# Optimization experiments

Measured on AMD Instinct MI355X. Metric: run time of the kernel, lower is better.

Reference implementation:

```python
import jax, jax.numpy as jnp
import numpy as np

HEADS = 8


def setup_inputs() -> dict:
    key = jax.random.key(0)
    ks = jax.random.split(key, 9)
    B, C, H, W = 16, 512, 32, 32
    d = C // HEADS
    scale = d ** -0.5
    return {
        "x": jax.random.normal(ks[0], (B, C, H, W), dtype=jnp.float32),
        "Wq": jax.random.normal(ks[1], (C, C), dtype=jnp.float32) * (C ** -0.5),
        "bq": jax.random.normal(ks[2], (C,), dtype=jnp.float32) * 0.02,
        "Wk": jax.random.normal(ks[3], (C, C), dtype=jnp.float32) * (C ** -0.5),
        "bk": jax.random.normal(ks[4], (C,), dtype=jnp.float32) * 0.02,
        "Wv": jax.random.normal(ks[5], (C, C), dtype=jnp.float32) * (C ** -0.5),
        "bv": jax.random.normal(ks[6], (C,), dtype=jnp.float32) * 0.02,
        "rel_h": jax.random.normal(ks[7], (d, H, 1), dtype=jnp.float32) * scale,
        "rel_w": jax.random.normal(ks[8], (d, 1, W), dtype=jnp.float32) * scale,
    }


def reference(x, Wq, bq, Wk, bk, Wv, bv, rel_h, rel_w):
    B, C, H, W = x.shape
    heads = HEADS
    d = C // heads
    scale = d ** -0.5
    N = H * W
    xf = x.reshape(B, C, N)  # 1x1 conv == per-pixel linear over channels
    q = (jnp.einsum('oc,bcn->bon', Wq, xf) + bq[:, None]).reshape(B, heads, d, N)
    k = (jnp.einsum('oc,bcn->bon', Wk, xf) + bk[:, None]).reshape(B, heads, d, N)
    v = (jnp.einsum('oc,bcn->bon', Wv, xf) + bv[:, None]).reshape(B, heads, d, N)
    q = q * scale
    # content-content scores [B, heads, N, N]
    cc = jnp.einsum('bhdi,bhdj->bhij', q, k)
    # relative position bias table [d, N], projected by q
    cp_tab = (rel_h + rel_w).reshape(d, N)
    cp = jnp.einsum('bhdi,dj->bhij', q, cp_tab)
    beta = jax.nn.softmax(cc + cp, axis=-1)
    attn = jnp.einsum('bhij,bhdj->bhid', beta, v)  # [B, heads, N, d]
    # original does .view(x.shape) on [b,h,i,d] -> keep same raw reshape
    return attn.reshape(B, C, H, W)
```

## Files before the change

kernel.cpp:

```cpp
#include <hip/hip_runtime.h>
#include <hip/hip_bf16.h>
#include <stdint.h>

typedef unsigned short u16;
typedef u16 u16x8 __attribute__((ext_vector_type(8)));
typedef u16 u16x4 __attribute__((ext_vector_type(4)));
typedef __bf16 bf16x8 __attribute__((ext_vector_type(8)));
typedef float f32x4 __attribute__((ext_vector_type(4)));

#define MFMA16(a, b, c) __builtin_amdgcn_mfma_f32_16x16x32_bf16((a), (b), (c), 0, 0, 0)

#define SCALE_Q 0.18033688011112042f

__device__ __forceinline__ u16 f2b(float f) {
    union { float f; unsigned u; } v; v.f = f;
    unsigned r = v.u + 0x7FFFu + ((v.u >> 16) & 1u);
    return (u16)(r >> 16);
}
__device__ __forceinline__ u16 f2b_h(float f) {
    union { float f; unsigned u; } v; v.f = f;
    return (u16)((v.u + 0x8000u) >> 16);
}

__device__ __forceinline__ void gload16(const u16* g, u16* l) {
    __builtin_amdgcn_global_load_lds(
        (const __attribute__((address_space(1))) unsigned int*)g,
        (__attribute__((address_space(3))) unsigned int*)l, 16, 0, 0);
}

__global__ __launch_bounds__(256) void prep(
    const float* __restrict__ x,
    const float* __restrict__ Wq, const float* __restrict__ Wk,
    const float* __restrict__ Wv,
    u16* __restrict__ wb, u16* __restrict__ xT) {
    __shared__ __align__(16) u16 Ls[128 * 72];
    const int tid = threadIdx.x;

    if (blockIdx.x < 384) {
        int g = blockIdx.x * 256 + tid;
        int which = g >> 15;
        const float* src = which == 0 ? Wq : (which == 1 ? Wk : Wv);
        int off = (g & 32767) * 8;
        f32x4 a = *(const f32x4*)(src + off);
        f32x4 b = *(const f32x4*)(src + off + 4);
        u16x8 o;
#pragma unroll
        for (int i = 0; i < 4; ++i) { o[i] = f2b_h(a[i]); o[4 + i] = f2b_h(b[i]); }
        *(u16x8*)(wb + (size_t)g * 8) = o;
        return;
    }

    const int bid = blockIdx.x - 384;
    const int b  = bid >> 6;
    const int ct = (bid >> 3) & 7;
    const int nt = bid & 7;
    const int C0 = ct * 64, N0 = nt * 128;
    const float* xb = x + ((size_t)b << 19);

#pragma unroll
    for (int rep = 0; rep < 4; ++rep) {
        int id = tid + rep * 256;
        int oct = id >> 7, n = id & 127;
        const float* xp = xb + (size_t)(C0 + oct * 8) * 1024 + N0 + n;
        u16x8 xv;
#pragma unroll
        for (int k = 0; k < 8; ++k) xv[k] = f2b_h(xp[k * 1024]);
        *(u16x8*)(Ls + n * 72 + oct * 8) = xv;
    }
    __syncthreads();
#pragma unroll
    for (int rep = 0; rep < 4; ++rep) {
        int id = tid + rep * 256;
        int n = id >> 3, c8 = id & 7;
        *(u16x8*)(xT + ((size_t)b << 19) + (size_t)(N0 + n) * 512 + C0 + c8 * 8) =
            *(u16x8*)(Ls + n * 72 + c8 * 8);
    }
}

__global__ __launch_bounds__(256, 3) void qkv_proj(
    const u16* __restrict__ xT, const u16* __restrict__ wb,
    const float* __restrict__ bq, const float* __restrict__ bk,
    const float* __restrict__ bv,
    const float* __restrict__ rel_h, const float* __restrict__ rel_w,
    u16* __restrict__ qws, u16* __restrict__ kws, u16* __restrict__ vws) {
    __shared__ __align__(16) u16 Xs[128 * 72];
    __shared__ __align__(16) u16 Ws[128 * 72];

    const int tid  = threadIdx.x;
    const int wave = tid >> 6, lane = tid & 63;
    const int quad = lane >> 4, l16 = lane & 15;
    const int wr = wave >> 1, wc = wave & 1;

    const int id = blockIdx.x;
    const int nt = id & 7;
    const int r  = id >> 3;
    const int o0 = r & 3;
    const int r2 = r >> 2;
    const int mm = r2 % 3;
    const int b  = r2 / 3;
    const int N0 = nt * 128;
    const int O0 = o0 * 128;

    const u16*   W    = wb + (size_t)mm * 262144;
    const float* bias = mm == 0 ? bq : (mm == 1 ? bk : bv);
    const u16*   Xb   = xT + ((size_t)b << 19);

    const int sr = tid >> 3, sc8 = tid & 7;

    u16x8 xr[4], wrg[4];
#pragma unroll
    for (int rp = 0; rp < 4; ++rp) {
        xr[rp]  = *(const u16x8*)(Xb + (size_t)(N0 + sr + rp * 32) * 512 + sc8 * 8);
        wrg[rp] = *(const u16x8*)(W  + (size_t)(O0 + sr + rp * 32) * 512 + sc8 * 8);
    }

    f32x4 acc[4][4] = {};

    for (int kt = 0; kt < 8; ++kt) {
        __syncthreads();
#pragma unroll
        for (int rp = 0; rp < 4; ++rp) {
            *(u16x8*)(Xs + (sr + rp * 32) * 72 + sc8 * 8) = xr[rp];
            *(u16x8*)(Ws + (sr + rp * 32) * 72 + sc8 * 8) = wrg[rp];
        }
        __syncthreads();
        if (kt < 7) {
            int c0 = (kt + 1) * 64;
#pragma unroll
            for (int rp = 0; rp < 4; ++rp) {
                xr[rp]  = *(const u16x8*)(Xb + (size_t)(N0 + sr + rp * 32) * 512 + c0 + sc8 * 8);
                wrg[rp] = *(const u16x8*)(W  + (size_t)(O0 + sr + rp * 32) * 512 + c0 + sc8 * 8);
            }
        }
#pragma unroll
        for (int kk = 0; kk < 2; ++kk) {
            bf16x8 af[4], bfr[4];
#pragma unroll
            for (int mi = 0; mi < 4; ++mi)
                af[mi] = *(bf16x8*)(Xs + (wr * 64 + mi * 16 + l16) * 72 + kk * 32 + quad * 8);
#pragma unroll
            for (int ni = 0; ni < 4; ++ni)
                bfr[ni] = *(bf16x8*)(Ws + (wc * 64 + ni * 16 + l16) * 72 + kk * 32 + quad * 8);
#pragma unroll
            for (int mi = 0; mi < 4; ++mi)
#pragma unroll
                for (int ni = 0; ni < 4; ++ni)
                    acc[mi][ni] = MFMA16(af[mi], bfr[ni], acc[mi][ni]);
        }
    }

#pragma unroll
    for (int mi = 0; mi < 4; ++mi) {
#pragma unroll
        for (int ni = 0; ni < 4; ++ni) {
            int o  = O0 + wc * 64 + ni * 16 + l16;
            int h  = o >> 6, dd = o & 63;
            size_t bh = (size_t)b * 8 + h;
            float bv_ = bias[o];
            int n0 = N0 + wr * 64 + mi * 16 + quad * 4;
            if (mm == 2) {
                u16x4 pk;
#pragma unroll
                for (int rr = 0; rr < 4; ++rr) pk[rr] = f2b(acc[mi][ni][rr] + bv_);
                int qq = (n0 >> 2) & 3, ss = (n0 >> 4) & 1;
                int np = (n0 & ~31) | (qq * 8 + ss * 4);
                int slot = ((np >> 3) & 7) ^ (dd & 7);
                int np2 = (np & ~63) | (slot << 3) | (np & 7);
                *(u16x4*)(vws + (bh * 64 + dd) * 1024 + np2) = pk;
            } else if (mm == 0) {
#pragma unroll
                for (int rr = 0; rr < 4; ++rr)
                    qws[(bh * 1024 + (n0 + rr)) * 64 + dd] =
                        f2b((acc[mi][ni][rr] + bv_) * SCALE_Q);
            } else {
                float th = rel_h[dd * 32 + (n0 >> 5)];
                f32x4 tw = *(const f32x4*)(rel_w + dd * 32 + (n0 & 31));
#pragma unroll
                for (int rr = 0; rr < 4; ++rr) {
                    int n = n0 + rr;
                    int sdd = (((dd >> 3) ^ (n & 7)) << 3) | (dd & 7);
                    kws[(bh * 1024 + n) * 64 + sdd] =
                        f2b(acc[mi][ni][rr] + bv_ + th + tw[rr]);
                }
            }
        }
    }
}

__global__ __launch_bounds__(512, 6) void attn(
    const u16* __restrict__ qws, const u16* __restrict__ kws,
    const u16* __restrict__ vws, float* __restrict__ out) {
    __shared__ __align__(16) u16 KPb[2][64 * 64];
    __shared__ __align__(16) u16 Vtb[2][64 * 64];

    const int tid  = threadIdx.x;
    const int wave = tid >> 6, lane = tid & 63;
    const int quad = lane >> 4, l16 = lane & 15;
    const int id = blockIdx.x;
    const int h  = id & 7;
    const int qt = (id >> 3) & 7;
    const int b  = id >> 6;
    const size_t bh = (size_t)b * 8 + h;

    const u16* Q = qws + (bh * 1024 + (size_t)qt * 128) * 64;
    const u16* K = kws + bh * 65536;
    const u16* V = vws + bh * 65536;

    const int lrow = wave * 8 + (lane >> 3);
    const int lc8  = lane & 7;
    const u16* Kl = K + (size_t)lrow * 64 + lc8 * 8;
    const u16* Vl = V + ((size_t)lrow << 10) + lc8 * 8;
    u16* const KP0 = &KPb[0][0];
    u16* const Vt0 = &Vtb[0][0];
    const int wofs = wave * 512;

    bf16x8 qf[2];
#pragma unroll
    for (int ks = 0; ks < 2; ++ks)
        qf[ks] = *(const bf16x8*)(Q + (wave * 16 + l16) * 64 + ks * 32 + quad * 8);

    const int xsw = (l16 & 7) << 4;
    const int xk0 = (quad * 16) ^ xsw;
    const int xk1 = (64 + quad * 16) ^ xsw;

    f32x4 accO[4] = {};
    f32x4 s4 = {};

    gload16(Kl, KP0 + wofs);
    gload16(Vl, Vt0 + wofs);

    auto body = [&](int jt, int cur) {
        __syncthreads();
        if (jt < 15) {
            int nxt = cur ^ 1;
            gload16(Kl + (jt + 1) * 4096, KP0 + nxt * 4096 + wofs);
            gload16(Vl + (jt + 1) * 64,  Vt0 + nxt * 4096 + wofs);
        }
        const char* KP = (const char*)(KP0 + cur * 4096);
        const char* Vt = (const char*)(Vt0 + cur * 4096);

        f32x4 accST[4] = {};
#pragma unroll
        for (int ks = 0; ks < 2; ++ks) {
            const int xo = ks ? xk1 : xk0;
            bf16x8 kf[4];
#pragma unroll
            for (int mj = 0; mj < 4; ++mj)
                kf[mj] = *(const bf16x8*)(KP + (mj * 16 + l16) * 128 + xo);
            __builtin_amdgcn_s_setprio(1);
#pragma unroll
            for (int mj = 0; mj < 4; ++mj)
                accST[mj] = MFMA16(kf[mj], qf[ks], accST[mj]);
            __builtin_amdgcn_s_setprio(0);
        }

#pragma unroll
        for (int mj = 0; mj < 4; ++mj) {
            f32x4 p;
#pragma unroll
            for (int rr = 0; rr < 4; ++rr)
                p[rr] = __builtin_amdgcn_exp2f(accST[mj][rr]);
            s4 += p;
            accST[mj] = p;
        }

#pragma unroll
        for (int ks2 = 0; ks2 < 2; ++ks2) {
            union { u16x8 u; bf16x8 b; } pfr;
            u16x8 t;
#pragma unroll
            for (int rr = 0; rr < 4; ++rr) {
                t[rr]     = f2b_h(accST[2 * ks2][rr]);
                t[4 + rr] = f2b_h(accST[2 * ks2 + 1][rr]);
            }
            pfr.u = t;
            const int xo = ks2 ? xk1 : xk0;
            bf16x8 vf[4];
#pragma unroll
            for (int md = 0; md < 4; ++md)
                vf[md] = *(const bf16x8*)(Vt + (md * 16 + l16) * 128 + xo);
            __builtin_amdgcn_s_setprio(1);
#pragma unroll
            for (int md = 0; md < 4; ++md)
                accO[md] = MFMA16(vf[md], pfr.b, accO[md]);
            __builtin_amdgcn_s_setprio(0);
        }
    };

    for (int j2 = 0; j2 < 8; ++j2) {
        body(2 * j2,     0);
        body(2 * j2 + 1, 1);
    }

    float rs = (s4[0] + s4[1]) + (s4[2] + s4[3]);
    rs += __shfl_xor(rs, 16);
    rs += __shfl_xor(rs, 32);
    float inv = 1.0f / rs;
    int i = qt * 128 + wave * 16 + l16;
#pragma unroll
    for (int md = 0; md < 4; ++md) {
        f32x4 pk;
#pragma unroll
        for (int rr = 0; rr < 4; ++rr) pk[rr] = accO[md][rr] * inv;
        *(f32x4*)(out + (bh * 1024 + i) * 64 + md * 16 + quad * 4) = pk;
    }
}

extern "C" void kernel_launch(void* const* d_in, const int* in_sizes, int n_in,
                              void* d_out, int out_size, void* d_ws, size_t ws_size,
                              hipStream_t stream) {
    const float* x  = (const float*)d_in[0];
    const float* Wq = (const float*)d_in[1];
    const float* bq = (const float*)d_in[2];
    const float* Wk = (const float*)d_in[3];
    const float* bk = (const float*)d_in[4];
    const float* Wv = (const float*)d_in[5];
    const float* bv = (const float*)d_in[6];
    const float* rh = (const float*)d_in[7];
    const float* rw = (const float*)d_in[8];
    float* out = (float*)d_out;

    u16* kws = (u16*)d_ws;
    u16* vws = kws + 8388608;
    u16* qws = vws + 8388608;
    u16* wb  = qws + 8388608;
    u16* xT  = (u16*)d_out;

    prep<<<1408, 256, 0, stream>>>(x, Wq, Wk, Wv, wb, xT);
    qkv_proj<<<1536, 256, 0, stream>>>(xT, wb, bq, bk, bv, rh, rw, qws, kws, vws);
    attn<<<1024, 512, 0, stream>>>(qws, kws, vws, out);
}
```

Before: 185.0 us.

## Double-buffer QKV GEMM via direct-to-LDS loads and double attention query tile

The QKV projection now streams 32-wide K slices straight into double-buffered, swizzled LDS with global_load_lds, replacing the register-staged copy and dropping one barrier per step. Its occupancy hint rises from 3 to 4 blocks. The attention kernel gives each wave 32 query rows instead of 16, so every K/V tile loaded into LDS is reused twice and the grid halves. P is packed to bf16 with the hardware v_cvt_pk_bf16_f32 instruction. The cost is higher register pressure in attn (occupancy hint lowered to 4) and fewer blocks to fill the GPU.

```diff
diff --git a/kernel.cpp b/kernel.cpp
--- a/kernel.cpp
+++ b/kernel.cpp
@@ -5,6 +5,7 @@
 typedef unsigned short u16;
 typedef u16 u16x8 __attribute__((ext_vector_type(8)));
 typedef u16 u16x4 __attribute__((ext_vector_type(4)));
+typedef unsigned int u32x4 __attribute__((ext_vector_type(4)));
 typedef __bf16 bf16x8 __attribute__((ext_vector_type(8)));
 typedef float f32x4 __attribute__((ext_vector_type(4)));
 
@@ -20,6 +21,11 @@
 __device__ __forceinline__ u16 f2b_h(float f) {
     union { float f; unsigned u; } v; v.f = f;
     return (u16)((v.u + 0x8000u) >> 16);
+}
+__device__ __forceinline__ unsigned pk2(float lo, float hi) {
+    unsigned r;
+    asm("v_cvt_pk_bf16_f32 %0, %1, %2" : "=v"(r) : "v"(lo), "v"(hi));
+    return r;
 }
 
 __device__ __forceinline__ void gload16(const u16* g, u16* l) {
@@ -77,14 +83,14 @@
     }
 }
 
-__global__ __launch_bounds__(256, 3) void qkv_proj(
+__global__ __launch_bounds__(256, 4) void qkv_proj(
     const u16* __restrict__ xT, const u16* __restrict__ wb,
     const float* __restrict__ bq, const float* __restrict__ bk,
     const float* __restrict__ bv,
     const float* __restrict__ rel_h, const float* __restrict__ rel_w,
     u16* __restrict__ qws, u16* __restrict__ kws, u16* __restrict__ vws) {
-    __shared__ __align__(16) u16 Xs[128 * 72];
-    __shared__ __align__(16) u16 Ws[128 * 72];
+    __shared__ __align__(16) u16 Xs2[2][128 * 32];
+    __shared__ __align__(16) u16 Ws2[2][128 * 32];
 
     const int tid  = threadIdx.x;
     const int wave = tid >> 6, lane = tid & 63;
@@ -105,48 +111,50 @@
     const float* bias = mm == 0 ? bq : (mm == 1 ? bk : bv);
     const u16*   Xb   = xT + ((size_t)b << 19);
 
-    const int sr = tid >> 3, sc8 = tid & 7;
-
-    u16x8 xr[4], wrg[4];
-#pragma unroll
-    for (int rp = 0; rp < 4; ++rp) {
-        xr[rp]  = *(const u16x8*)(Xb + (size_t)(N0 + sr + rp * 32) * 512 + sc8 * 8);
-        wrg[rp] = *(const u16x8*)(W  + (size_t)(O0 + sr + rp * 32) * 512 + sc8 * 8);
-    }
+    const int srow = wave * 16 + (lane >> 2);
+    const int sl   = ((lane & 3) ^ (lane >> 4)) * 8;
+    const u16* Xg = Xb + (size_t)(N0 + srow) * 512 + sl;
+    const u16* Wg = W  + (size_t)(O0 + srow) * 512 + sl;
+    u16* const XL = &Xs2[0][0];
+    u16* const WL = &Ws2[0][0];
+    const int wofs = wave * 512;
+
+    auto STAGE = [&](int kt, int buf) {
+        gload16(Xg + kt * 32,         XL + buf * 4096 + wofs);
+        gload16(Xg + kt * 32 + 32768, XL + buf * 4096 + 2048 + wofs);
+        gload16(Wg + kt * 32,         WL + buf * 4096 + wofs);
+        gload16(Wg + kt * 32 + 32768, WL + buf * 4096 + 2048 + wofs);
+    };
 
     f32x4 acc[4][4] = {};
-
-    for (int kt = 0; kt < 8; ++kt) {
+    const int fsl = (quad ^ (l16 >> 2)) * 8;
+
+    STAGE(0, 0);
+
+    auto step = [&](int kt, int cur) {
         __syncthreads();
-#pragma unroll
-        for (int rp = 0; rp < 4; ++rp) {
-            *(u16x8*)(Xs + (sr + rp * 32) * 72 + sc8 * 8) = xr[rp];
-            *(u16x8*)(Ws + (sr + rp * 32) * 72 + sc8 * 8) = wrg[rp];
-        }
-        __syncthreads();
-        if (kt < 7) {
-            int c0 = (kt + 1) * 64;
-#pragma unroll
-            for (int rp = 0; rp < 4; ++rp) {
-                xr[rp]  = *(const u16x8*)(Xb + (size_t)(N0 + sr + rp * 32) * 512 + c0 + sc8 * 8);
-                wrg[rp] = *(const u16x8*)(W  + (size_t)(O0 + sr + rp * 32) * 512 + c0 + sc8 * 8);
-            }
-        }
-#pragma unroll
-        for (int kk = 0; kk < 2; ++kk) {
-            bf16x8 af[4], bfr[4];
-#pragma unroll
-            for (int mi = 0; mi < 4; ++mi)
-                af[mi] = *(bf16x8*)(Xs + (wr * 64 + mi * 16 + l16) * 72 + kk * 32 + quad * 8);
+        if (kt < 15) STAGE(kt + 1, cur ^ 1);
+        const u16* Xc = XL + cur * 4096;
+        const u16* Wc = WL + cur * 4096;
+        bf16x8 af[4], bfr[4];
+#pragma unroll
+        for (int mi = 0; mi < 4; ++mi)
+            af[mi] = *(const bf16x8*)(Xc + (wr * 64 + mi * 16 + l16) * 32 + fsl);
+#pragma unroll
+        for (int ni = 0; ni < 4; ++ni)
+            bfr[ni] = *(const bf16x8*)(Wc + (wc * 64 + ni * 16 + l16) * 32 + fsl);
+        __builtin_amdgcn_s_setprio(1);
+#pragma unroll
+        for (int mi = 0; mi < 4; ++mi)
 #pragma unroll
             for (int ni = 0; ni < 4; ++ni)
-                bfr[ni] = *(bf16x8*)(Ws + (wc * 64 + ni * 16 + l16) * 72 + kk * 32 + quad * 8);
-#pragma unroll
-            for (int mi = 0; mi < 4; ++mi)
-#pragma unroll
-                for (int ni = 0; ni < 4; ++ni)
-                    acc[mi][ni] = MFMA16(af[mi], bfr[ni], acc[mi][ni]);
-        }
+                acc[mi][ni] = MFMA16(af[mi], bfr[ni], acc[mi][ni]);
+        __builtin_amdgcn_s_setprio(0);
+    };
+
+    for (int k2 = 0; k2 < 8; ++k2) {
+        step(2 * k2,     0);
+        step(2 * k2 + 1, 1);
     }
 
 #pragma unroll
@@ -187,7 +195,7 @@
     }
 }
 
-__global__ __launch_bounds__(512, 6) void attn(
+__global__ __launch_bounds__(512, 4) void attn(
     const u16* __restrict__ qws, const u16* __restrict__ kws,
     const u16* __restrict__ vws, float* __restrict__ out) {
     __shared__ __align__(16) u16 KPb[2][64 * 64];
@@ -198,11 +206,11 @@
     const int quad = lane >> 4, l16 = lane & 15;
     const int id = blockIdx.x;
     const int h  = id & 7;
-    const int qt = (id >> 3) & 7;
-    const int b  = id >> 6;
+    const int qt = (id >> 3) & 3;
+    const int b  = id >> 5;
     const size_t bh = (size_t)b * 8 + h;
 
-    const u16* Q = qws + (bh * 1024 + (size_t)qt * 128) * 64;
+    const u16* Q = qws + (bh * 1024 + (size_t)qt * 256) * 64;
     const u16* K = kws + bh * 65536;
     const u16* V = vws + bh * 65536;
 
@@ -214,17 +222,19 @@
     u16* const Vt0 = &Vtb[0][0];
     const int wofs = wave * 512;
 
-    bf16x8 qf[2];
-#pragma unroll
-    for (int ks = 0; ks < 2; ++ks)
-        qf[ks] = *(const bf16x8*)(Q + (wave * 16 + l16) * 64 + ks * 32 + quad * 8);
+    bf16x8 qf[2][2];
+#pragma unroll
+    for (int ni = 0; ni < 2; ++ni)
+#pragma unroll
+        for (int ks = 0; ks < 2; ++ks)
+            qf[ni][ks] = *(const bf16x8*)(Q + (wave * 32 + ni * 16 + l16) * 64 + ks * 32 + quad * 8);
 
     const int xsw = (l16 & 7) << 4;
     const int xk0 = (quad * 16) ^ xsw;
     const int xk1 = (64 + quad * 16) ^ xsw;
 
-    f32x4 accO[4] = {};
-    f32x4 s4 = {};
+    f32x4 accO[4][2] = {};
+    f32x4 s4[2] = {};
 
     gload16(Kl, KP0 + wofs);
     gload16(Vl, Vt0 + wofs);
@@ -239,7 +249,7 @@
         const char* KP = (const char*)(KP0 + cur * 4096);
         const char* Vt = (const char*)(Vt0 + cur * 4096);
 
-        f32x4 accST[4] = {};
+        f32x4 aST[4][2] = {};
 #pragma unroll
         for (int ks = 0; ks < 2; ++ks) {
             const int xo = ks ? xk1 : xk0;
@@ -250,30 +260,34 @@
             __builtin_amdgcn_s_setprio(1);
 #pragma unroll
             for (int mj = 0; mj < 4; ++mj)
-                accST[mj] = MFMA16(kf[mj], qf[ks], accST[mj]);
+#pragma unroll
+                for (int ni = 0; ni < 2; ++ni)
+                    aST[mj][ni] = MFMA16(kf[mj], qf[ni][ks], aST[mj][ni]);
             __builtin_amdgcn_s_setprio(0);
         }
 
 #pragma unroll
-        for (int mj = 0; mj < 4; ++mj) {
-            f32x4 p;
-#pragma unroll
-            for (int rr = 0; rr < 4; ++rr)
-                p[rr] = __builtin_amdgcn_exp2f(accST[mj][rr]);
-            s4 += p;
-            accST[mj] = p;
-        }
+        for (int mj = 0; mj < 4; ++mj)
+#pragma unroll
+            for (int ni = 0; ni < 2; ++ni) {
+                f32x4 p;
+#pragma unroll
+                for (int rr = 0; rr < 4; ++rr)
+                    p[rr] = __builtin_amdgcn_exp2f(aST[mj][ni][rr]);
+                s4[ni] += p;
+                aST[mj][ni] = p;
+            }
 
 #pragma unroll
         for (int ks2 = 0; ks2 < 2; ++ks2) {
-            union { u16x8 u; bf16x8 b; } pfr;
-            u16x8 t;
-#pragma unroll
-            for (int rr = 0; rr < 4; ++rr) {
-                t[rr]     = f2b_h(accST[2 * ks2][rr]);
-                t[4 + rr] = f2b_h(accST[2 * ks2 + 1][rr]);
+            union { u32x4 u; bf16x8 b; } pfr[2];
+#pragma unroll
+            for (int ni = 0; ni < 2; ++ni) {
+                pfr[ni].u[0] = pk2(aST[2 * ks2][ni][0],     aST[2 * ks2][ni][1]);
+                pfr[ni].u[1] = pk2(aST[2 * ks2][ni][2],     aST[2 * ks2][ni][3]);
+                pfr[ni].u[2] = pk2(aST[2 * ks2 + 1][ni][0], aST[2 * ks2 + 1][ni][1]);
+                pfr[ni].u[3] = pk2(aST[2 * ks2 + 1][ni][2], aST[2 * ks2 + 1][ni][3]);
             }
-            pfr.u = t;
             const int xo = ks2 ? xk1 : xk0;
             bf16x8 vf[4];
 #pragma unroll
@@ -282,7 +296,9 @@
             __builtin_amdgcn_s_setprio(1);
 #pragma unroll
             for (int md = 0; md < 4; ++md)
-                accO[md] = MFMA16(vf[md], pfr.b, accO[md]);
+#pragma unroll
+                for (int ni = 0; ni < 2; ++ni)
+                    accO[md][ni] = MFMA16(vf[md], pfr[ni].b, accO[md][ni]);
             __builtin_amdgcn_s_setprio(0);
         }
     };
@@ -292,17 +308,20 @@
         body(2 * j2 + 1, 1);
     }
 
-    float rs = (s4[0] + s4[1]) + (s4[2] + s4[3]);
-    rs += __shfl_xor(rs, 16);
-    rs += __shfl_xor(rs, 32);
-    float inv = 1.0f / rs;
-    int i = qt * 128 + wave * 16 + l16;
-#pragma unroll
-    for (int md = 0; md < 4; ++md) {
-        f32x4 pk;
-#pragma unroll
-        for (int rr = 0; rr < 4; ++rr) pk[rr] = accO[md][rr] * inv;
-        *(f32x4*)(out + (bh * 1024 + i) * 64 + md * 16 + quad * 4) = pk;
+#pragma unroll
+    for (int ni = 0; ni < 2; ++ni) {
+        float rs = (s4[ni][0] + s4[ni][1]) + (s4[ni][2] + s4[ni][3]);
+        rs += __shfl_xor(rs, 16);
+        rs += __shfl_xor(rs, 32);
+        float inv = 1.0f / rs;
+        int i = qt * 256 + wave * 32 + ni * 16 + l16;
+#pragma unroll
+        for (int md = 0; md < 4; ++md) {
+            f32x4 pk;
+#pragma unroll
+            for (int rr = 0; rr < 4; ++rr) pk[rr] = accO[md][ni][rr] * inv;
+            *(f32x4*)(out + (bh * 1024 + i) * 64 + md * 16 + quad * 4) = pk;
+        }
     }
 }
 
@@ -328,5 +347,5 @@
 
     prep<<<1408, 256, 0, stream>>>(x, Wq, Wk, Wv, wb, xT);
     qkv_proj<<<1536, 256, 0, stream>>>(xT, wb, bq, bk, bv, rh, rw, qws, kws, vws);
-    attn<<<1024, 512, 0, stream>>>(qws, kws, vws, out);
-}
+    attn<<<512, 512, 0, stream>>>(qws, kws, vws, out);
+}
```

New measurement: 184.7 us. No clear change (-0.1%).
